# Kernel optimization log

Hardware: AMD Instinct MI355X
Metric: run time of the kernel (lower is better)

The kernel has to match this reference:

```python
import jax, jax.numpy as jnp
import numpy as np

BN_EPS = 1e-5

def _bn(y, g, b, m, v):
    # inference-mode BatchNorm2d over channel axis 1
    return (y - m[:, None, None]) * (g[:, None, None] / jnp.sqrt(v[:, None, None] + BN_EPS)) + b[:, None, None]

def setup_inputs() -> dict:
    key = jax.random.key(0)
    ks = jax.random.split(key, 16)
    B, C, H, W = 16, 128, 128, 128
    E, O = 256, 128
    inp = {
        'x1': jax.random.normal(ks[0], (B, C, H, W), jnp.float32),
        'x2': jax.random.normal(ks[1], (B, C, H, W), jnp.float32),
        # conv1: 1x1 Conv2d(C -> E)
        'w1': jax.random.normal(ks[2], (E, C), jnp.float32) * (1.0 / np.sqrt(C)),
        'b1': jax.random.normal(ks[3], (E,), jnp.float32) * 0.01,
        'g1': jax.random.uniform(ks[4], (E,), jnp.float32, 0.5, 1.5),
        'beta1': jax.random.normal(ks[5], (E,), jnp.float32) * 0.01,
        'm1': jax.random.normal(ks[6], (E,), jnp.float32) * 0.01,
        'v1': jax.random.uniform(ks[7], (E,), jnp.float32, 0.5, 1.5),
        # conv2: 1x1 Conv2d(E -> O)
        'w2': jax.random.normal(ks[8], (O, E), jnp.float32) * (1.0 / np.sqrt(E)),
        'b2': jax.random.normal(ks[9], (O,), jnp.float32) * 0.01,
        'g2': jax.random.uniform(ks[10], (O,), jnp.float32, 0.5, 1.5),
        'beta2': jax.random.normal(ks[11], (O,), jnp.float32) * 0.01,
        'm2': jax.random.normal(ks[12], (O,), jnp.float32) * 0.01,
        'v2': jax.random.uniform(ks[13], (O,), jnp.float32, 0.5, 1.5),
    }
    return inp

def _fft_atten(t, w1, b1, g1, beta1, m1, v1, w2, b2, g2, beta2, m2, v2):
    y = jnp.einsum('bchw,ec->behw', t, w1) + b1[:, None, None]
    y = jax.nn.relu(_bn(y, g1, beta1, m1, v1))
    y = jnp.einsum('behw,oe->bohw', y, w2) + b2[:, None, None]
    return _bn(y, g2, beta2, m2, v2)

def reference(x1, x2, w1, b1, g1, beta1, m1, v1, w2, b2, g2, beta2, m2, v2):
    b, c, h, w = x2.shape
    R = (h + w) // 32
    # vectorized high-pass mask (replaces the per-pixel Python loop)
    yy = (jnp.arange(h, dtype=x2.dtype) - (h - 1) / 2.0) ** 2
    xx = (jnp.arange(w, dtype=x2.dtype) - (w - 1) / 2.0) ** 2
    hpf = (yy[:, None] + xx[None, :] >= float(R * R)).astype(x2.dtype)  # [h,w]
    f = jnp.fft.fftn(x2, axes=(2, 3), norm='ortho')
    f = jnp.fft.fftshift(f)  # torch default shifts ALL axes, incl. batch/channel
    hf = f * hpf
    real = hf.real + _fft_atten(hf.real, w1, b1, g1, beta1, m1, v1, w2, b2, g2, beta2, m2, v2)
    imag = hf.imag + _fft_atten(hf.imag, w1, b1, g1, beta1, m1, v1, w2, b2, g2, beta2, m2, v2)
    hx = jnp.abs(jnp.fft.ifftn(jax.lax.complex(real, imag), s=x1.shape[-2:], axes=(2, 3), norm='ortho'))
    return (x1 * hx + x1, x2 * hx + x2, hx)
```

## Files before the change

### kernel.cpp

```cpp
#include <hip/hip_runtime.h>
#include <math.h>

#define PLANE 16384
#define NTOT  33554432u
typedef unsigned int  uint;
typedef unsigned short ushort;

typedef __attribute__((ext_vector_type(8))) short short8;
typedef __attribute__((ext_vector_type(8))) ushort ushort8;
typedef __attribute__((ext_vector_type(4))) float f32x4;

__device__ __forceinline__ ushort f2bf(float x){
  unsigned u = __float_as_uint(x);
  u = (u + 0x7FFFu + ((u >> 16) & 1u)) >> 16;
  return (ushort)u;
}
__device__ __forceinline__ float bf2f(ushort h){
  return __uint_as_float(((uint)h) << 16);
}
__device__ __forceinline__ uint pk(float a, float b){
  return (uint)f2bf(a) | ((uint)f2bf(b) << 16);
}

__device__ __forceinline__ int bitrev6(int x){
  return ((x&1)<<5)|((x&2)<<3)|((x&4)<<1)|((x&8)>>1)|((x&16)>>3)|((x&32)>>5);
}
__device__ __forceinline__ int rev4(int m){
  return ((m&1)<<3)|((m&2)<<1)|((m&4)>>1)|((m&8)>>3);
}
__device__ __forceinline__ float bperm(int srcLane, float v){
  return __int_as_float(__builtin_amdgcn_ds_bpermute(srcLane<<2, __float_as_int(v)));
}

template<int FWD, int PERM>
__device__ __forceinline__ void fft128(float& v0r, float& v0i, float& v1r, float& v1i, int l){
  const float SGN = FWD ? -3.14159265358979323846f : 3.14159265358979323846f;
  {
    float ar = v0r + v1r, ai = v0i + v1i;
    float br = v0r - v1r, bi = v0i - v1i;
    float ang = SGN * (float)l * (1.0f/64.0f);
    float s, c; __sincosf(ang, &s, &c);
    v0r = ar; v0i = ai;
    v1r = br*c - bi*s; v1i = br*s + bi*c;
  }
  #pragma unroll
  for(int h = 32; h >= 1; h >>= 1){
    int hi = l & h;
    int tt = hi ? (l & (h-1)) : 0;
    float ang = SGN * (float)tt / (float)h;
    float s, c; __sincosf(ang, &s, &c);
    float sg = hi ? -1.f : 1.f;
    float o_r = __shfl_xor(v0r, h), o_i = __shfl_xor(v0i, h);
    float dr = o_r + sg*v0r, di = o_i + sg*v0i;
    v0r = dr*c - di*s; v0i = dr*s + di*c;
    o_r = __shfl_xor(v1r, h); o_i = __shfl_xor(v1i, h);
    dr = o_r + sg*v1r; di = o_i + sg*v1i;
    v1r = dr*c - di*s; v1i = dr*s + di*c;
  }
  if(PERM){
    int L = bitrev6(l >> 1);
    float p0r = bperm(L,   v0r), p0i = bperm(L,   v0i);
    float q0r = bperm(L,   v1r), q0i = bperm(L,   v1i);
    float p1r = bperm(L+1, v0r), p1i = bperm(L+1, v0i);
    float q1r = bperm(L+1, v1r), q1i = bperm(L+1, v1i);
    if(l & 1){ v0r=q0r; v0i=q0i; v1r=q1r; v1i=q1i; }
    else     { v0r=p0r; v0i=p0i; v1r=p1r; v1i=p1i; }
  }
}

__global__ __launch_bounds__(256) void k_prep(
    const float* __restrict__ w1, const float* __restrict__ b1,
    const float* __restrict__ g1, const float* __restrict__ be1,
    const float* __restrict__ m1, const float* __restrict__ v1,
    const float* __restrict__ w2, const float* __restrict__ b2,
    const float* __restrict__ g2, const float* __restrict__ be2,
    const float* __restrict__ m2, const float* __restrict__ v2,
    float* __restrict__ wb){
  int g = blockIdx.x*256 + threadIdx.x;
  ushort* wbs = (ushort*)wb;
  if(g < 32768){
    int kt = (g >> 9) & 3, l = (g >> 3) & 63, j = g & 7;
    int et = g >> 11;
    int c = kt*32 + 8*(l>>4) + j;
    int e = et*16 + (l&15);
    float s1 = g1[e]*rsqrtf(v1[e]+1e-5f);
    wbs[g] = f2bf(w1[e*128 + c]*s1);
  } else {
    int g2i = g - 32768;
    int ot = g2i >> 12, kt = (g2i >> 9) & 7, l = (g2i >> 3) & 63, j = g2i & 7;
    int o = ot*16 + (l&15);
    int e = kt*32 + 8*(l>>4) + j;
    float s2 = g2[o]*rsqrtf(v2[o]+1e-5f);
    wbs[32768 + g2i] = f2bf(w2[o*256 + e]*s2);
  }
  if(g < 256){
    float s1 = g1[g]*rsqrtf(v1[g]+1e-5f);
    wb[32768 + g] = b1[g]*s1 + be1[g] - m1[g]*s1;
  }
  if(g < 128){
    float s2 = g2[g]*rsqrtf(v2[g]+1e-5f);
    wb[33024 + g] = b2[g]*s2 + be2[g] - m2[g]*s2;
  }
}

__global__ __launch_bounds__(512) void k_fft_fwd(const float* __restrict__ x2,
                                                 uint* __restrict__ spec){
  __shared__ float sRe[32*129];
  __shared__ float sIm[32*129];
  int bid = blockIdx.x;
  int b = bid >> 7, c = bid & 127;
  int tid = threadIdx.x, wv = tid >> 6, l = tid & 63;
  const float* src = x2 + (size_t)(b*128 + c)*PLANE;
  float R0r[16], R0i[16], R1r[16], R1i[16];
  #pragma unroll
  for(int i=0;i<16;i++){
    int r = wv*16 + i;
    float a  = src[r*128 + l];
    float bb = src[r*128 + l + 64];
    float v0r=a, v0i=0.f, v1r=bb, v1i=0.f;
    fft128<1,0>(v0r,v0i,v1r,v1i,l);
    R0r[i]=v0r; R0i[i]=v0i; R1r[i]=v1r; R1i[i]=v1i;
  }
  int bp = (b + 8) & 15, cp = (c + 64) & 127;
  uint* dst = spec + (size_t)(bp*128 + cp)*PLANE;
  const float SC = 1.0f/128.0f;
  int wq = rev4(l>>2) << 1;
  for(int s4=0; s4<4; s4++){
    __syncthreads();
    int r2 = ((s4&1)<<1) | ((s4>>1)&1);
    if((l&3) == r2){
      #pragma unroll
      for(int i=0;i<16;i++){
        int r = wv*16 + i;
        sRe[wq*129 + r]     = R0r[i];  sIm[wq*129 + r]     = R0i[i];
        sRe[(wq+1)*129 + r] = R1r[i];  sIm[(wq+1)*129 + r] = R1i[i];
      }
    }
    __syncthreads();
    #pragma unroll
    for(int q=0;q<4;q++){
      int j = wv*4 + q;
      float v0r = sRe[j*129 + l],      v0i = sIm[j*129 + l];
      float v1r = sRe[j*129 + l + 64], v1i = sIm[j*129 + l + 64];
      fft128<1,1>(v0r,v0i,v1r,v1i,l);
      int w  = s4*32 + j;
      int wd = w ^ 64;
      float dwc = (float)wd - 63.5f;
      float dw2 = dwc*dwc;
      float d0 = (float)l        - 63.5f;
      float d1 = (float)(l + 64) - 63.5f;
      float m0 = (d0*d0 + dw2 >= 64.0f) ? SC : 0.0f;
      float m1 = (d1*d1 + dw2 >= 64.0f) ? SC : 0.0f;
      dst[wd*128 + l]      = pk(v1r*m0, v1i*m0);
      dst[wd*128 + l + 64] = pk(v0r*m1, v0i*m1);
    }
  }
}

#define XPITCH 136
#define EPITCH 264
__global__ __launch_bounds__(256,3) void k_conv(const float* __restrict__ wb,
                                                const uint* __restrict__ spec,
                                                uint* __restrict__ zo){
  __shared__ ushort xs[64*XPITCH];
  __shared__ ushort hs[64*EPITCH];
  const ushort* wbs = (const ushort*)wb;
  int bid = blockIdx.x;
  int b = bid >> 9;
  int pix0 = (bid & 511) * 32;
  const uint* sp = spec + (size_t)(b*128)*PLANE + pix0;
  int t = threadIdx.x, l = t & 63, w = t >> 6;

  {
    int p = t & 31, g = t >> 5;
    #pragma unroll
    for(int half=0; half<2; half++){
      ushort re8[8], im8[8];
      #pragma unroll
      for(int k=0;k<8;k++){
        uint u = sp[(size_t)(g*16 + half*8 + k)*PLANE + p];
        re8[k] = (ushort)u; im8[k] = (ushort)(u>>16);
      }
      *(ushort8*)(xs + p*XPITCH      + g*16 + half*8) = *(ushort8*)re8;
      *(ushort8*)(xs + (p+32)*XPITCH + g*16 + half*8) = *(ushort8*)im8;
    }
  }

  short8 bw1[4][4];
  #pragma unroll
  for(int et=0; et<4; et++)
    #pragma unroll
    for(int kt=0; kt<4; kt++)
      bw1[et][kt] = *(const short8*)(wbs + (((w*4+et)*4 + kt)*64 + l)*8);
  float c1v[4];
  #pragma unroll
  for(int et=0; et<4; et++) c1v[et] = wb[32768 + w*64 + et*16 + (l&15)];

  __syncthreads();

  #pragma unroll
  for(int mt=0; mt<4; mt++){
    short8 xa[4];
    #pragma unroll
    for(int kt=0; kt<4; kt++)
      xa[kt] = *(const short8*)(xs + (mt*16 + (l&15))*XPITCH + kt*32 + 8*(l>>4));
    f32x4 a0 = {0,0,0,0}, a1 = {0,0,0,0}, a2 = {0,0,0,0}, a3 = {0,0,0,0};
    #pragma unroll
    for(int kt=0; kt<4; kt++){
      a0 = __builtin_amdgcn_mfma_f32_16x16x32_bf16(xa[kt], bw1[0][kt], a0, 0,0,0);
      a1 = __builtin_amdgcn_mfma_f32_16x16x32_bf16(xa[kt], bw1[1][kt], a1, 0,0,0);
      a2 = __builtin_amdgcn_mfma_f32_16x16x32_bf16(xa[kt], bw1[2][kt], a2, 0,0,0);
      a3 = __builtin_amdgcn_mfma_f32_16x16x32_bf16(xa[kt], bw1[3][kt], a3, 0,0,0);
    }
    #pragma unroll
    for(int et=0; et<4; et++){
      f32x4 av = et==0?a0 : et==1?a1 : et==2?a2 : a3;
      #pragma unroll
      for(int r=0; r<4; r++){
        float h = fmaxf(av[r] + c1v[et], 0.f);
        hs[(mt*16 + (l>>4)*4 + r)*EPITCH + w*64 + et*16 + (l&15)] = f2bf(h);
      }
    }
  }

  short8 aw2[2][8];
  #pragma unroll
  for(int ot=0; ot<2; ot++)
    #pragma unroll
    for(int kt=0; kt<8; kt++)
      aw2[ot][kt] = *(const short8*)(wbs + 32768 + (((w*2+ot)*8 + kt)*64 + l)*8);
  float c2r[8];
  #pragma unroll
  for(int ot=0; ot<2; ot++)
    #pragma unroll
    for(int r=0; r<4; r++)
      c2r[ot*4+r] = wb[33024 + w*32 + ot*16 + (l>>4)*4 + r];

  __syncthreads();

  f32x4 d[2][4];
  #pragma unroll
  for(int ot=0; ot<2; ot++)
    #pragma unroll
    for(int pt=0; pt<4; pt++) d[ot][pt] = (f32x4){0,0,0,0};
  for(int kt=0; kt<8; kt++){
    short8 hb[4];
    #pragma unroll
    for(int pt=0; pt<4; pt++)
      hb[pt] = *(const short8*)(hs + (pt*16 + (l&15))*EPITCH + kt*32 + 8*(l>>4));
    #pragma unroll
    for(int ot=0; ot<2; ot++)
      #pragma unroll
      for(int pt=0; pt<4; pt++)
        d[ot][pt] = __builtin_amdgcn_mfma_f32_16x16x32_bf16(aw2[ot][kt], hb[pt], d[ot][pt], 0,0,0);
  }

  uint* zb = zo + (size_t)(b*128)*PLANE + pix0;
  #pragma unroll
  for(int ot=0; ot<2; ot++){
    #pragma unroll
    for(int pp=0; pp<2; pp++){
      #pragma unroll
      for(int r=0; r<4; r++){
        int o = w*32 + ot*16 + (l>>4)*4 + r;
        int p = pp*16 + (l&15);
        float re = d[ot][pp][r]   + c2r[ot*4+r] + bf2f(xs[p*XPITCH + o]);
        float im = d[ot][pp+2][r] + c2r[ot*4+r] + bf2f(xs[(p+32)*XPITCH + o]);
        zb[(size_t)o*PLANE + p] = pk(re, im);
      }
    }
  }
}

__global__ __launch_bounds__(512) void k_ifft_out(const uint* z,
                                                  const float* __restrict__ xin1,
                                                  const float* __restrict__ xin2,
                                                  float* out){
  __shared__ float sRe[32*129];
  __shared__ float sIm[32*129];
  int bid = blockIdx.x;
  int b = bid >> 7, o = bid & 127;
  size_t plane = (size_t)(b*128 + o)*PLANE;
  const uint* zp = z + plane;
  int tid = threadIdx.x, wv = tid >> 6, l = tid & 63;
  float R0r[16], R0i[16], R1r[16], R1i[16];
  #pragma unroll
  for(int i=0;i<16;i++){
    int r = wv*16 + i;
    uint u0 = zp[r*128 + l], u1 = zp[r*128 + l + 64];
    float v0r = bf2f((ushort)u0), v0i = bf2f((ushort)(u0>>16));
    float v1r = bf2f((ushort)u1), v1i = bf2f((ushort)(u1>>16));
    fft128<0,0>(v0r,v0i,v1r,v1i,l);
    R0r[i]=v0r; R0i[i]=v0i; R1r[i]=v1r; R1i[i]=v1i;
  }
  const float SC = 1.0f/128.0f;
  int wq = rev4(l>>2) << 1;
  for(int s4=0; s4<4; s4++){
    __syncthreads();
    int r2 = ((s4&1)<<1) | ((s4>>1)&1);
    if((l&3) == r2){
      #pragma unroll
      for(int i=0;i<16;i++){
        int r = wv*16 + i;
        sRe[wq*129 + r]     = R0r[i];  sIm[wq*129 + r]     = R0i[i];
        sRe[(wq+1)*129 + r] = R1r[i];  sIm[(wq+1)*129 + r] = R1i[i];
      }
    }
    __syncthreads();
    #pragma unroll
    for(int q=0;q<4;q++){
      int j = wv*4 + q;
      float v0r = sRe[j*129 + l],      v0i = sIm[j*129 + l];
      float v1r = sRe[j*129 + l + 64], v1i = sIm[j*129 + l + 64];
      fft128<0,1>(v0r,v0i,v1r,v1i,l);
      int nh = s4*32 + j;
      float h0 = sqrtf(v0r*v0r + v0i*v0i) * SC;
      float h1 = sqrtf(v1r*v1r + v1i*v1i) * SC;
      size_t i0 = plane + (size_t)nh*128 + l, i1 = i0 + 64;
      float u = xin1[i0], v = xin2[i0];
      out[i0] = u*h0 + u;  out[NTOT + i0] = v*h0 + v;  out[2u*NTOT + i0] = h0;
      u = xin1[i1]; v = xin2[i1];
      out[i1] = u*h1 + u;  out[NTOT + i1] = v*h1 + v;  out[2u*NTOT + i1] = h1;
    }
  }
}

extern "C" void kernel_launch(void* const* d_in, const int* in_sizes, int n_in,
                              void* d_out, int out_size, void* d_ws, size_t ws_size,
                              hipStream_t stream){
  (void)in_sizes; (void)n_in; (void)d_ws; (void)ws_size; (void)out_size;
  const float* x1  = (const float*)d_in[0];
  const float* x2  = (const float*)d_in[1];
  const float* w1  = (const float*)d_in[2];
  const float* b1  = (const float*)d_in[3];
  const float* g1  = (const float*)d_in[4];
  const float* be1 = (const float*)d_in[5];
  const float* m1  = (const float*)d_in[6];
  const float* v1  = (const float*)d_in[7];
  const float* w2  = (const float*)d_in[8];
  const float* b2  = (const float*)d_in[9];
  const float* g2  = (const float*)d_in[10];
  const float* be2 = (const float*)d_in[11];
  const float* m2  = (const float*)d_in[12];
  const float* v2  = (const float*)d_in[13];
  float* out = (float*)d_out;
  float* wb   = out;
  uint*  spec = (uint*)(out + NTOT);
  uint*  z    = (uint*)(out + 2u*NTOT);
  hipLaunchKernelGGL(k_prep,     dim3(256),  dim3(256), 0, stream,
                     w1,b1,g1,be1,m1,v1,w2,b2,g2,be2,m2,v2, wb);
  hipLaunchKernelGGL(k_fft_fwd,  dim3(2048), dim3(512), 0, stream, x2, spec);
  hipLaunchKernelGGL(k_conv,     dim3(8192), dim3(256), 0, stream, wb, spec, z);
  hipLaunchKernelGGL(k_ifft_out, dim3(2048), dim3(512), 0, stream, z, x1, x2, out);
}
```

Before: 517.3 us.

## Replace shuffle-based radix-2 FFTs with bf16 MFMA DFT matrix multiplies

Both the forward and inverse 2D FFT kernels drop the wave-shuffle butterfly FFTs and compute each 128-point transform as a dense DFT matmul on MFMA bf16 units. The twiddle matrices are generated per block in shared memory, and the row pass is double-buffered with prefetch of the next 16-row slab. The aim is to move FFT arithmetic off the shuffle and transcendental path onto matrix cores. In exchange it does O(N^2) work instead of O(N log N), uses a large shared-memory footprint that limits the kernel to one block per CU, and loses accuracy from bf16 twiddles and intermediates.

```diff
diff --git a/kernel.cpp b/kernel.cpp
--- a/kernel.cpp
+++ b/kernel.cpp
@@ -3,12 +3,15 @@
 
 #define PLANE 16384
 #define NTOT  33554432u
+#define TP    136
 typedef unsigned int  uint;
 typedef unsigned short ushort;
 
-typedef __attribute__((ext_vector_type(8))) short short8;
+typedef __attribute__((ext_vector_type(8))) short  short8;
 typedef __attribute__((ext_vector_type(8))) ushort ushort8;
-typedef __attribute__((ext_vector_type(4))) float f32x4;
+typedef __attribute__((ext_vector_type(4))) ushort bf16x4;
+typedef __attribute__((ext_vector_type(4))) uint   u32x4;
+typedef __attribute__((ext_vector_type(4))) float  f32x4;
 
 __device__ __forceinline__ ushort f2bf(float x){
   unsigned u = __float_as_uint(x);
@@ -22,49 +25,23 @@
   return (uint)f2bf(a) | ((uint)f2bf(b) << 16);
 }
 
-__device__ __forceinline__ int bitrev6(int x){
-  return ((x&1)<<5)|((x&2)<<3)|((x&4)<<1)|((x&8)>>1)|((x&16)>>3)|((x&32)>>5);
-}
-__device__ __forceinline__ int rev4(int m){
-  return ((m&1)<<3)|((m&2)<<1)|((m&4)>>1)|((m&8)>>3);
-}
-__device__ __forceinline__ float bperm(int srcLane, float v){
-  return __int_as_float(__builtin_amdgcn_ds_bpermute(srcLane<<2, __float_as_int(v)));
-}
-
-template<int FWD, int PERM>
-__device__ __forceinline__ void fft128(float& v0r, float& v0i, float& v1r, float& v1i, int l){
-  const float SGN = FWD ? -3.14159265358979323846f : 3.14159265358979323846f;
-  {
-    float ar = v0r + v1r, ai = v0i + v1i;
-    float br = v0r - v1r, bi = v0i - v1i;
-    float ang = SGN * (float)l * (1.0f/64.0f);
-    float s, c; __sincosf(ang, &s, &c);
-    v0r = ar; v0i = ai;
-    v1r = br*c - bi*s; v1i = br*s + bi*c;
-  }
-  #pragma unroll
-  for(int h = 32; h >= 1; h >>= 1){
-    int hi = l & h;
-    int tt = hi ? (l & (h-1)) : 0;
-    float ang = SGN * (float)tt / (float)h;
-    float s, c; __sincosf(ang, &s, &c);
-    float sg = hi ? -1.f : 1.f;
-    float o_r = __shfl_xor(v0r, h), o_i = __shfl_xor(v0i, h);
-    float dr = o_r + sg*v0r, di = o_i + sg*v0i;
-    v0r = dr*c - di*s; v0i = dr*s + di*c;
-    o_r = __shfl_xor(v1r, h); o_i = __shfl_xor(v1i, h);
-    dr = o_r + sg*v1r; di = o_i + sg*v1i;
-    v1r = dr*c - di*s; v1i = dr*s + di*c;
-  }
-  if(PERM){
-    int L = bitrev6(l >> 1);
-    float p0r = bperm(L,   v0r), p0i = bperm(L,   v0i);
-    float q0r = bperm(L,   v1r), q0i = bperm(L,   v1i);
-    float p1r = bperm(L+1, v0r), p1i = bperm(L+1, v0i);
-    float q1r = bperm(L+1, v1r), q1i = bperm(L+1, v1i);
-    if(l & 1){ v0r=q0r; v0i=q0i; v1r=q1r; v1i=q1i; }
-    else     { v0r=p0r; v0i=p0i; v1r=p1r; v1i=p1i; }
+template<int SGN>
+__device__ __forceinline__ void gen_table(ushort* Fre, ushort* Fim, int t){
+  int n = t >> 2, kb = (t & 3) * 32;
+  #pragma unroll
+  for(int q=0; q<4; q++){
+    ushort8 cv, sv;
+    #pragma unroll
+    for(int j=0; j<8; j++){
+      int k = kb + q*8 + j;
+      int idx = (n*k) & 127;
+      float ss, cc;
+      __sincosf((float)idx * 0.049087385212340517f, &ss, &cc);
+      cv[j] = f2bf(cc);
+      sv[j] = f2bf(SGN < 0 ? -ss : ss);
+    }
+    *(ushort8*)(&Fre[n*TP + kb + q*8]) = cv;
+    *(ushort8*)(&Fim[n*TP + kb + q*8]) = sv;
   }
 }
 
@@ -103,56 +80,90 @@
   }
 }
 
-__global__ __launch_bounds__(512) void k_fft_fwd(const float* __restrict__ x2,
-                                                 uint* __restrict__ spec){
-  __shared__ float sRe[32*129];
-  __shared__ float sIm[32*129];
-  int bid = blockIdx.x;
-  int b = bid >> 7, c = bid & 127;
-  int tid = threadIdx.x, wv = tid >> 6, l = tid & 63;
+__global__ __launch_bounds__(512,1) void k_fft_fwd(const float* __restrict__ x2,
+                                                   uint* __restrict__ spec){
+  __shared__ ushort Fre[128*TP], Fim[128*TP];
+  __shared__ ushort Pre[128*TP], Pim[128*TP];
+  __shared__ ushort xb[2][16*TP];
+  int t = threadIdx.x, l = t & 63, wv = t >> 6;
+  int bid = blockIdx.x, b = bid >> 7, c = bid & 127;
   const float* src = x2 + (size_t)(b*128 + c)*PLANE;
-  float R0r[16], R0i[16], R1r[16], R1i[16];
-  #pragma unroll
-  for(int i=0;i<16;i++){
-    int r = wv*16 + i;
-    float a  = src[r*128 + l];
-    float bb = src[r*128 + l + 64];
-    float v0r=a, v0i=0.f, v1r=bb, v1i=0.f;
-    fft128<1,0>(v0r,v0i,v1r,v1i,l);
-    R0r[i]=v0r; R0i[i]=v0i; R1r[i]=v1r; R1i[i]=v1i;
+  gen_table<-1>(Fre, Fim, t);
+  int hr = t >> 5, c4 = (t & 31)*4;
+  {
+    f32x4 v = *(const f32x4*)(src + hr*128 + c4);
+    bf16x4 o;
+    #pragma unroll
+    for(int j=0;j<4;j++) o[j] = f2bf(v[j]);
+    *(bf16x4*)(&xb[0][hr*TP + c4]) = o;
+  }
+  __syncthreads();
+  int koff = 8*(l >> 4);
+  for(int s=0; s<8; s++){
+    f32x4 pf;
+    if(s < 7) pf = *(const f32x4*)(src + (16*(s+1) + hr)*128 + c4);
+    int arow = (l & 15)*TP;
+    int brow = (16*(wv ^ 4) + (l & 15))*TP;
+    f32x4 pr = {0,0,0,0}, pi = {0,0,0,0};
+    #pragma unroll
+    for(int kt=0; kt<4; kt++){
+      short8 xa = *(const short8*)(&xb[s&1][arow + kt*32 + koff]);
+      short8 fr = *(const short8*)(&Fre[brow + kt*32 + koff]);
+      short8 fi = *(const short8*)(&Fim[brow + kt*32 + koff]);
+      pr = __builtin_amdgcn_mfma_f32_16x16x32_bf16(xa, fr, pr, 0,0,0);
+      pi = __builtin_amdgcn_mfma_f32_16x16x32_bf16(xa, fi, pi, 0,0,0);
+    }
+    int wd = 16*wv + (l & 15);
+    int hb = 16*s + 4*(l >> 4);
+    bf16x4 pr4, pi4;
+    #pragma unroll
+    for(int r=0;r<4;r++){ pr4[r] = f2bf(pr[r]); pi4[r] = f2bf(pi[r]); }
+    *(bf16x4*)(&Pre[wd*TP + hb]) = pr4;
+    *(bf16x4*)(&Pim[wd*TP + hb]) = pi4;
+    if(s < 7){
+      bf16x4 o;
+      #pragma unroll
+      for(int j=0;j<4;j++) o[j] = f2bf(pf[j]);
+      *(bf16x4*)(&xb[(s+1)&1][hr*TP + c4]) = o;
+    }
+    __syncthreads();
   }
   int bp = (b + 8) & 15, cp = (c + 64) & 127;
   uint* dst = spec + (size_t)(bp*128 + cp)*PLANE;
+  int arow2 = (16*wv + (l & 15))*TP;
+  short8 ar[4], ai[4];
+  #pragma unroll
+  for(int kt=0; kt<4; kt++){
+    ar[kt] = *(const short8*)(&Pre[arow2 + kt*32 + koff]);
+    ai[kt] = *(const short8*)(&Pim[arow2 + kt*32 + koff]);
+  }
   const float SC = 1.0f/128.0f;
-  int wq = rev4(l>>2) << 1;
-  for(int s4=0; s4<4; s4++){
-    __syncthreads();
-    int r2 = ((s4&1)<<1) | ((s4>>1)&1);
-    if((l&3) == r2){
-      #pragma unroll
-      for(int i=0;i<16;i++){
-        int r = wv*16 + i;
-        sRe[wq*129 + r]     = R0r[i];  sIm[wq*129 + r]     = R0i[i];
-        sRe[(wq+1)*129 + r] = R1r[i];  sIm[(wq+1)*129 + r] = R1i[i];
-      }
-    }
-    __syncthreads();
-    #pragma unroll
-    for(int q=0;q<4;q++){
-      int j = wv*4 + q;
-      float v0r = sRe[j*129 + l],      v0i = sIm[j*129 + l];
-      float v1r = sRe[j*129 + l + 64], v1i = sIm[j*129 + l + 64];
-      fft128<1,1>(v0r,v0i,v1r,v1i,l);
-      int w  = s4*32 + j;
-      int wd = w ^ 64;
-      float dwc = (float)wd - 63.5f;
-      float dw2 = dwc*dwc;
-      float d0 = (float)l        - 63.5f;
-      float d1 = (float)(l + 64) - 63.5f;
-      float m0 = (d0*d0 + dw2 >= 64.0f) ? SC : 0.0f;
-      float m1 = (d1*d1 + dw2 >= 64.0f) ? SC : 0.0f;
-      dst[wd*128 + l]      = pk(v1r*m0, v1i*m0);
-      dst[wd*128 + l + 64] = pk(v0r*m1, v0i*m1);
+  #pragma unroll
+  for(int ct=0; ct<8; ct++){
+    int brow = (16*(ct ^ 4) + (l & 15))*TP;
+    f32x4 sr_ = {0,0,0,0}, si_ = {0,0,0,0};
+    #pragma unroll
+    for(int kt=0; kt<4; kt++){
+      short8 fi = *(const short8*)(&Fim[brow + kt*32 + koff]);
+      sr_ = __builtin_amdgcn_mfma_f32_16x16x32_bf16(ai[kt], fi, sr_, 0,0,0);
+      si_ = __builtin_amdgcn_mfma_f32_16x16x32_bf16(ar[kt], fi, si_, 0,0,0);
+    }
+    sr_ = -sr_;
+    #pragma unroll
+    for(int kt=0; kt<4; kt++){
+      short8 fr = *(const short8*)(&Fre[brow + kt*32 + koff]);
+      sr_ = __builtin_amdgcn_mfma_f32_16x16x32_bf16(ar[kt], fr, sr_, 0,0,0);
+      si_ = __builtin_amdgcn_mfma_f32_16x16x32_bf16(ai[kt], fr, si_, 0,0,0);
+    }
+    int hd = 16*ct + (l & 15);
+    float dh = (float)hd - 63.5f;
+    float dh2 = dh*dh;
+    #pragma unroll
+    for(int r=0; r<4; r++){
+      int wd = 16*wv + 4*(l>>4) + r;
+      float dw = (float)wd - 63.5f;
+      float m = (dw*dw + dh2 >= 64.0f) ? SC : 0.0f;
+      dst[wd*128 + hd] = pk(sr_[r]*m, si_[r]*m);
     }
   }
 }
@@ -170,7 +181,6 @@
   int pix0 = (bid & 511) * 32;
   const uint* sp = spec + (size_t)(b*128)*PLANE + pix0;
   int t = threadIdx.x, l = t & 63, w = t >> 6;
-
   {
     int p = t & 31, g = t >> 5;
     #pragma unroll
@@ -185,7 +195,6 @@
       *(ushort8*)(xs + (p+32)*XPITCH + g*16 + half*8) = *(ushort8*)im8;
     }
   }
-
   short8 bw1[4][4];
   #pragma unroll
   for(int et=0; et<4; et++)
@@ -195,9 +204,7 @@
   float c1v[4];
   #pragma unroll
   for(int et=0; et<4; et++) c1v[et] = wb[32768 + w*64 + et*16 + (l&15)];
-
   __syncthreads();
-
   #pragma unroll
   for(int mt=0; mt<4; mt++){
     short8 xa[4];
@@ -222,7 +229,6 @@
       }
     }
   }
-
   short8 aw2[2][8];
   #pragma unroll
   for(int ot=0; ot<2; ot++)
@@ -235,9 +241,7 @@
     #pragma unroll
     for(int r=0; r<4; r++)
       c2r[ot*4+r] = wb[33024 + w*32 + ot*16 + (l>>4)*4 + r];
-
   __syncthreads();
-
   f32x4 d[2][4];
   #pragma unroll
   for(int ot=0; ot<2; ot++)
@@ -254,7 +258,6 @@
       for(int pt=0; pt<4; pt++)
         d[ot][pt] = __builtin_amdgcn_mfma_f32_16x16x32_bf16(aw2[ot][kt], hb[pt], d[ot][pt], 0,0,0);
   }
-
   uint* zb = zo + (size_t)(b*128)*PLANE + pix0;
   #pragma unroll
   for(int ot=0; ot<2; ot++){
@@ -272,55 +275,104 @@
   }
 }
 
-__global__ __launch_bounds__(512) void k_ifft_out(const uint* z,
-                                                  const float* __restrict__ xin1,
-                                                  const float* __restrict__ xin2,
-                                                  float* out){
-  __shared__ float sRe[32*129];
-  __shared__ float sIm[32*129];
-  int bid = blockIdx.x;
-  int b = bid >> 7, o = bid & 127;
+__global__ __launch_bounds__(512,1) void k_ifft_out(const uint* z,
+                                                    const float* __restrict__ xin1,
+                                                    const float* __restrict__ xin2,
+                                                    float* out){
+  __shared__ ushort Gre[128*TP], Gim[128*TP];
+  __shared__ ushort Tre[128*TP], Tim[128*TP];
+  __shared__ ushort zbr[2][16*TP], zbi[2][16*TP];
+  int t = threadIdx.x, l = t & 63, wv = t >> 6;
+  int bid = blockIdx.x, b = bid >> 7, o = bid & 127;
   size_t plane = (size_t)(b*128 + o)*PLANE;
   const uint* zp = z + plane;
-  int tid = threadIdx.x, wv = tid >> 6, l = tid & 63;
-  float R0r[16], R0i[16], R1r[16], R1i[16];
-  #pragma unroll
-  for(int i=0;i<16;i++){
-    int r = wv*16 + i;
-    uint u0 = zp[r*128 + l], u1 = zp[r*128 + l + 64];
-    float v0r = bf2f((ushort)u0), v0i = bf2f((ushort)(u0>>16));
-    float v1r = bf2f((ushort)u1), v1i = bf2f((ushort)(u1>>16));
-    fft128<0,0>(v0r,v0i,v1r,v1i,l);
-    R0r[i]=v0r; R0i[i]=v0i; R1r[i]=v1r; R1i[i]=v1i;
+  gen_table<1>(Gre, Gim, t);
+  int rr = t >> 5, c4 = (t & 31)*4;
+  {
+    u32x4 u = *(const u32x4*)(zp + rr*128 + c4);
+    bf16x4 ur, ui;
+    #pragma unroll
+    for(int j=0;j<4;j++){ ur[j] = (ushort)u[j]; ui[j] = (ushort)(u[j]>>16); }
+    *(bf16x4*)(&zbr[0][rr*TP + c4]) = ur;
+    *(bf16x4*)(&zbi[0][rr*TP + c4]) = ui;
+  }
+  __syncthreads();
+  int koff = 8*(l >> 4);
+  for(int s=0; s<8; s++){
+    u32x4 pf;
+    if(s < 7) pf = *(const u32x4*)(zp + (16*(s+1) + rr)*128 + c4);
+    int arow = (l & 15)*TP;
+    int brow = (16*wv + (l & 15))*TP;
+    short8 zr[4], zi[4], gr[4], gi[4];
+    #pragma unroll
+    for(int kt=0; kt<4; kt++){
+      zr[kt] = *(const short8*)(&zbr[s&1][arow + kt*32 + koff]);
+      zi[kt] = *(const short8*)(&zbi[s&1][arow + kt*32 + koff]);
+      gr[kt] = *(const short8*)(&Gre[brow + kt*32 + koff]);
+      gi[kt] = *(const short8*)(&Gim[brow + kt*32 + koff]);
+    }
+    f32x4 tr = {0,0,0,0}, ti = {0,0,0,0};
+    #pragma unroll
+    for(int kt=0; kt<4; kt++) tr = __builtin_amdgcn_mfma_f32_16x16x32_bf16(zi[kt], gi[kt], tr, 0,0,0);
+    tr = -tr;
+    #pragma unroll
+    for(int kt=0; kt<4; kt++) tr = __builtin_amdgcn_mfma_f32_16x16x32_bf16(zr[kt], gr[kt], tr, 0,0,0);
+    #pragma unroll
+    for(int kt=0; kt<4; kt++){
+      ti = __builtin_amdgcn_mfma_f32_16x16x32_bf16(zr[kt], gi[kt], ti, 0,0,0);
+      ti = __builtin_amdgcn_mfma_f32_16x16x32_bf16(zi[kt], gr[kt], ti, 0,0,0);
+    }
+    int nh = 16*wv + (l & 15);
+    int wdb = 16*s + 4*(l >> 4);
+    bf16x4 t4r, t4i;
+    #pragma unroll
+    for(int r=0;r<4;r++){ t4r[r] = f2bf(tr[r]); t4i[r] = f2bf(ti[r]); }
+    *(bf16x4*)(&Tre[nh*TP + wdb]) = t4r;
+    *(bf16x4*)(&Tim[nh*TP + wdb]) = t4i;
+    if(s < 7){
+      bf16x4 ur, ui;
+      #pragma unroll
+      for(int j=0;j<4;j++){ ur[j] = (ushort)pf[j]; ui[j] = (ushort)(pf[j]>>16); }
+      *(bf16x4*)(&zbr[(s+1)&1][rr*TP + c4]) = ur;
+      *(bf16x4*)(&zbi[(s+1)&1][rr*TP + c4]) = ui;
+    }
+    __syncthreads();
+  }
+  int arow2 = (16*wv + (l & 15))*TP;
+  short8 ar[4], ai[4];
+  #pragma unroll
+  for(int kt=0; kt<4; kt++){
+    ar[kt] = *(const short8*)(&Tre[arow2 + kt*32 + koff]);
+    ai[kt] = *(const short8*)(&Tim[arow2 + kt*32 + koff]);
   }
   const float SC = 1.0f/128.0f;
-  int wq = rev4(l>>2) << 1;
-  for(int s4=0; s4<4; s4++){
-    __syncthreads();
-    int r2 = ((s4&1)<<1) | ((s4>>1)&1);
-    if((l&3) == r2){
-      #pragma unroll
-      for(int i=0;i<16;i++){
-        int r = wv*16 + i;
-        sRe[wq*129 + r]     = R0r[i];  sIm[wq*129 + r]     = R0i[i];
-        sRe[(wq+1)*129 + r] = R1r[i];  sIm[(wq+1)*129 + r] = R1i[i];
-      }
-    }
-    __syncthreads();
-    #pragma unroll
-    for(int q=0;q<4;q++){
-      int j = wv*4 + q;
-      float v0r = sRe[j*129 + l],      v0i = sIm[j*129 + l];
-      float v1r = sRe[j*129 + l + 64], v1i = sIm[j*129 + l + 64];
-      fft128<0,1>(v0r,v0i,v1r,v1i,l);
-      int nh = s4*32 + j;
-      float h0 = sqrtf(v0r*v0r + v0i*v0i) * SC;
-      float h1 = sqrtf(v1r*v1r + v1i*v1i) * SC;
-      size_t i0 = plane + (size_t)nh*128 + l, i1 = i0 + 64;
-      float u = xin1[i0], v = xin2[i0];
-      out[i0] = u*h0 + u;  out[NTOT + i0] = v*h0 + v;  out[2u*NTOT + i0] = h0;
-      u = xin1[i1]; v = xin2[i1];
-      out[i1] = u*h1 + u;  out[NTOT + i1] = v*h1 + v;  out[2u*NTOT + i1] = h1;
+  #pragma unroll
+  for(int ct=0; ct<8; ct++){
+    int brow = (16*ct + (l & 15))*TP;
+    f32x4 sr_ = {0,0,0,0}, si_ = {0,0,0,0};
+    #pragma unroll
+    for(int kt=0; kt<4; kt++){
+      short8 gi = *(const short8*)(&Gim[brow + kt*32 + koff]);
+      sr_ = __builtin_amdgcn_mfma_f32_16x16x32_bf16(ai[kt], gi, sr_, 0,0,0);
+      si_ = __builtin_amdgcn_mfma_f32_16x16x32_bf16(ar[kt], gi, si_, 0,0,0);
+    }
+    sr_ = -sr_;
+    #pragma unroll
+    for(int kt=0; kt<4; kt++){
+      short8 gr = *(const short8*)(&Gre[brow + kt*32 + koff]);
+      sr_ = __builtin_amdgcn_mfma_f32_16x16x32_bf16(ar[kt], gr, sr_, 0,0,0);
+      si_ = __builtin_amdgcn_mfma_f32_16x16x32_bf16(ai[kt], gr, si_, 0,0,0);
+    }
+    #pragma unroll
+    for(int r=0; r<4; r++){
+      int nh = 16*wv + 4*(l>>4) + r;
+      int nw = 16*ct + (l & 15);
+      size_t idx = plane + (size_t)nh*128 + nw;
+      float h = sqrtf(sr_[r]*sr_[r] + si_[r]*si_[r]) * SC;
+      float u = xin1[idx], v = xin2[idx];
+      out[idx] = u*h + u;
+      out[NTOT + idx] = v*h + v;
+      out[2u*NTOT + idx] = h;
     }
   }
 }
```

Measured after the change: 426.1 us. 1.21x faster.
